# Kernel tuning notes

Hardware: AMD Instinct MI355X
Metric: run time of the kernel (lower is better)

## Reference

```python
import jax, jax.numpy as jnp
import numpy as np

N = 1048576
N_GRID = 256
DX = 1.0 / N_GRID
INV_DX = float(N_GRID)
DT = 2e-5
P_VOL = (DX * 0.5) ** 2
P_RHO = 1.0
P_MASS = P_VOL * P_RHO
E_MOD = 1000.0
NU = 0.2
MU_0 = E_MOD / (2.0 * (1.0 + NU))
LAM_0 = E_MOD * NU / ((1.0 + NU) * (1.0 - 2.0 * NU))
GRAVITY = 50.0


def setup_inputs() -> dict:
    key = jax.random.key(0)
    k = jax.random.split(key, 5)
    x = 0.1 + 0.8 * jax.random.uniform(k[0], (N, 2), dtype=jnp.float32)
    v = 0.1 * jax.random.normal(k[1], (N, 2), dtype=jnp.float32)
    C = 0.5 * jax.random.normal(k[2], (N, 2, 2), dtype=jnp.float32)
    F = jnp.eye(2, dtype=jnp.float32)[None] + 0.1 * jax.random.normal(k[3], (N, 2, 2), dtype=jnp.float32)
    material = jax.random.randint(k[4], (N,), 0, 3, dtype=jnp.int32)
    Jp = jnp.ones((N,), dtype=jnp.float32)
    return {"x": x, "v": v, "C": C, "F": F, "material": material, "Jp": Jp}


def reference(x, v, C, F, material, Jp):
    dt, inv_dx, dx = DT, INV_DX, DX
    base = jnp.floor(x * inv_dx - 0.5).astype(jnp.int32)          # [N,2]
    fx = x * inv_dx - base.astype(x.dtype)                        # [N,2]
    # quadratic B-spline weights, stacked over the 3 taps -> [3,N,2]
    w = jnp.stack([0.5 * (1.5 - fx) ** 2,
                   0.75 - (fx - 1.0) ** 2,
                   0.5 * (fx - 0.5) ** 2], axis=0)

    # deformation gradient update
    F = F + dt * jnp.einsum('nij,njk->nik', C, F)

    h = jnp.exp(10.0 * (1.0 - Jp))
    h = jnp.where(material == 1, 0.3, h)
    mu = jnp.where(material == 0, 0.0, MU_0 * h)
    lam = LAM_0 * h

    # per-particle 2x2 SVD (original pads to 3x3 and slices back)
    U, sig, Vh = jnp.linalg.svd(F)

    # snow plasticity: clamp singular values, track Jp
    clamped = jnp.clip(sig, 1.0 - 2.5e-2, 1.0 + 4.5e-3)
    is_snow = material == 2
    Jp = jnp.where(is_snow, Jp * jnp.prod(sig / clamped, axis=-1), Jp)
    sig = jnp.where(is_snow[:, None], clamped, sig)

    J = jnp.prod(sig, axis=-1)
    eye2 = jnp.eye(2, dtype=x.dtype)
    F_fluid = eye2[None] * jnp.sqrt(J)[:, None, None]             # J^(1/n_dim), n_dim=2
    F_snow = jnp.einsum('nij,nj,njk->nik', U, sig, Vh)
    F = jnp.where((material == 0)[:, None, None], F_fluid,
                  jnp.where(is_snow[:, None, None], F_snow, F))

    R = jnp.einsum('nij,njk->nik', U, Vh)
    stress = (2.0 * mu[:, None, None] * jnp.einsum('nij,nkj->nik', F - R, F)
              + eye2[None] * (lam * J * (J - 1.0))[:, None, None])
    stress = (-dt * P_VOL * 4.0 * inv_dx ** 2) * stress
    affine = stress + P_MASS * C                                   # [N,2,2]

    # ---- P2G scatter over the 3x3 stencil (vectorized over 9 taps) ----
    offs = jnp.array([[i, j] for i in range(3) for j in range(3)], dtype=jnp.int32)  # [9,2]
    weight = w[offs[:, 0], :, 0] * w[offs[:, 1], :, 1]             # [9,N]
    target = base[None, :, :] + offs[:, None, :]                   # [9,N,2]
    idx = target[..., 0] * N_GRID + target[..., 1]                 # [9,N]
    flat_idx = idx.reshape(-1)
    NG2 = N_GRID * N_GRID

    v_add = P_MASS * v - jnp.einsum('nij,nj->ni', affine, x)       # [N,2]
    grid_v = jax.ops.segment_sum((weight[..., None] * v_add[None]).reshape(-1, 2),
                                 flat_idx, num_segments=NG2).reshape(N_GRID, N_GRID, 2)
    grid_affine = jax.ops.segment_sum((weight[..., None, None] * affine[None]).reshape(-1, 4),
                                      flat_idx, num_segments=NG2).reshape(N_GRID, N_GRID, 2, 2)
    grid_m = jax.ops.segment_sum((weight * P_MASS).reshape(-1),
                                 flat_idx, num_segments=NG2).reshape(N_GRID, N_GRID)

    grid_x = jnp.stack(jnp.meshgrid(jnp.arange(N_GRID), jnp.arange(N_GRID), indexing='ij'),
                       axis=-1).astype(x.dtype) * dx               # [G,G,2]
    grid_v = grid_v + jnp.einsum('abij,abj->abi', grid_affine, grid_x)

    # grid ops: momentum -> velocity, gravity, boundary clamps
    m = grid_m[..., None]
    grid_v = jnp.where(m > 0, grid_v / jnp.maximum(m, 1e-12), grid_v)
    grid_v = grid_v.at[:, :, 1].add(-dt * GRAVITY)
    grid_v = grid_v.at[:3, :, 0].max(0.0)
    grid_v = grid_v.at[-2:, :, 0].min(0.0)
    grid_v = grid_v.at[:, :3, 1].max(0.0)
    grid_v = grid_v.at[:, -2:, 1].min(0.0)

    # ---- G2P gather ----
    gvf = grid_v.reshape(NG2, 2)
    g_v = gvf[idx]                                                 # [9,N,2]
    new_v = jnp.sum(weight[..., None] * g_v, axis=0)               # [N,2]
    pos = target.astype(x.dtype) * dx                              # [9,N,2]
    new_C = jnp.sum(weight[..., None, None] * g_v[..., :, None] * pos[..., None, :], axis=0)
    new_C = (new_C - new_v[..., None] * x[:, None, :]) * (4.0 * inv_dx ** 2)

    x = x + dt * new_v
    return (x, new_v, new_C, F, material, Jp)
```

## Files before the change

kernel.cpp:

```cpp
#include <hip/hip_runtime.h>

#define NG 256
#define NG2 (NG*NG)
#define NREP 8

constexpr float DX      = 1.0f / 256.0f;
constexpr float INV_DX  = 256.0f;
constexpr float DT      = 2e-5f;
constexpr float P_VOL   = (1.0f/512.0f) * (1.0f/512.0f);
constexpr float P_MASS  = P_VOL;
constexpr float MU_0    = 1000.0f / (2.0f * 1.2f);
constexpr float LAM_0   = 1000.0f * 0.2f / (1.2f * 0.6f);
constexpr float GRAV    = 50.0f;

__device__ __forceinline__ int bin_of(float px, float py) {
    int bx = (int)floorf(px * INV_DX - 0.5f);
    int by = (int)floorf(py * INV_DX - 0.5f);
    bx = min(max(bx, 0), NG - 1);
    by = min(max(by, 0), NG - 1);
    return (bx << 8) | by;
}

__device__ __forceinline__ float bw(float t) {
    float at = fabsf(t);
    float a  = fmaxf(1.5f - at, 0.0f);
    float w1 = 0.75f - t * t;
    float w2 = 0.5f * a * a;
    return (at < 0.5f) ? w1 : w2;
}


__global__ __launch_bounds__(256) void binrank_kernel(
    const float* __restrict__ x, int* __restrict__ counts8,
    unsigned char* __restrict__ rank, int n)
{
    int i = blockIdx.x * blockDim.x + threadIdx.x;
    if (i >= n) return;
    float2 p = ((const float2*)x)[i];
    int b = bin_of(p.x, p.y);
    int rep = (i >> 8) & (NREP - 1);
    rank[i] = (unsigned char)atomicAdd(&counts8[rep * NG2 + b], 1);
}

__global__ __launch_bounds__(256) void scan1_kernel(
    const int* __restrict__ counts8, uint2* __restrict__ offs8,
    int* __restrict__ starts, int* __restrict__ bsum)
{
    __shared__ int tmp[256];
    int t = threadIdx.x, blk = blockIdx.x;
    int b = blk * 256 + t;

    int c0 = counts8[0*NG2 + b], c1 = counts8[1*NG2 + b];
    int c2 = counts8[2*NG2 + b], c3 = counts8[3*NG2 + b];
    int c4 = counts8[4*NG2 + b], c5 = counts8[5*NG2 + b];
    int c6 = counts8[6*NG2 + b], c7 = counts8[7*NG2 + b];
    int o1 = c0, o2 = o1+c1, o3 = o2+c2, o4 = o3+c3;
    int o5 = o4+c4, o6 = o5+c5, o7 = o6+c6;
    int total = o7 + c7;
    uint2 packed;
    packed.x = (unsigned)(o1 << 8) | ((unsigned)o2 << 16) | ((unsigned)o3 << 24);
    packed.y = (unsigned)o4 | ((unsigned)o5 << 8) | ((unsigned)o6 << 16) | ((unsigned)o7 << 24);
    offs8[b] = packed;

    tmp[t] = total;
    __syncthreads();
    #pragma unroll
    for (int off = 1; off < 256; off <<= 1) {
        int add = (t >= off) ? tmp[t - off] : 0;
        __syncthreads();
        tmp[t] += add;
        __syncthreads();
    }
    starts[b] = tmp[t] - total;
    if (t == 255) bsum[blk] = tmp[255];
}

__global__ __launch_bounds__(256) void scan2_kernel(int* __restrict__ bsum)
{
    __shared__ int tmp[256];
    int t = threadIdx.x;
    int v = bsum[t];
    tmp[t] = v;
    __syncthreads();
    #pragma unroll
    for (int off = 1; off < 256; off <<= 1) {
        int add = (t >= off) ? tmp[t - off] : 0;
        __syncthreads();
        tmp[t] += add;
        __syncthreads();
    }
    bsum[t] = tmp[t] - v;
}

__global__ __launch_bounds__(256) void scan3_kernel(
    int* __restrict__ starts, const int* __restrict__ bsum, int n)
{
    int i = blockIdx.x * blockDim.x + threadIdx.x;
    if (i < NG2) starts[i] += bsum[i >> 8];
    if (i == 0) starts[NG2] = n;
}


__global__ __launch_bounds__(256) void compute_scatter_kernel(
    const float* __restrict__ x, const float* __restrict__ v,
    const float* __restrict__ C, const float* __restrict__ F,
    const int* __restrict__ mat, const float* __restrict__ Jp,
    const int* __restrict__ starts, const uint2* __restrict__ offs8,
    const unsigned char* __restrict__ rank,
    float4* __restrict__ srec,
    float4* __restrict__ F_out4, float* __restrict__ mat_out, float* __restrict__ Jp_out,
    int n)
{
    int i = blockIdx.x * blockDim.x + threadIdx.x;
    if (i >= n) return;

    float2 xp = ((const float2*)x)[i];
    float px = xp.x, py = xp.y;

    int bin = bin_of(px, py);
    int rep = (i >> 8) & (NREP - 1);
    uint2 o8 = offs8[bin];
    int sb = starts[bin];
    int rk = (int)rank[i];

    float2 vp = ((const float2*)v)[i];
    float4 Cp = ((const float4*)C)[i];
    float4 Fp = ((const float4*)F)[i];
    int    m  = mat[i];
    float  jp = Jp[i];

    float C00 = Cp.x, C01 = Cp.y, C10 = Cp.z, C11 = Cp.w;
    float a = Fp.x, b = Fp.y, c = Fp.z, d = Fp.w;

    float na = a + DT*(C00*a + C01*c);
    float nb = b + DT*(C00*b + C01*d);
    float nc = c + DT*(C10*a + C11*c);
    float nd = d + DT*(C10*b + C11*d);
    a = na; b = nb; c = nc; d = nd;

    float h = expf(10.0f * (1.0f - jp));
    if (m == 1) h = 0.3f;
    float mu  = (m == 0) ? 0.0f : MU_0 * h;
    float lam = LAM_0 * h;

    float S00 = a*a + c*c, S01 = a*b + c*d, S11 = b*b + d*d;
    float mh = 0.5f*(S00 + S11), dh = 0.5f*(S00 - S11);
    float delta = sqrtf(dh*dh + S01*S01);
    float sig1 = sqrtf(fmaxf(mh + delta, 0.0f));
    float sig2 = sqrtf(fmaxf(mh - delta, 0.0f));
    float e0, e1;
    if (dh >= 0.0f) { e0 = delta + dh; e1 = S01; }
    else            { e0 = S01;        e1 = delta - dh; }
    float elen = sqrtf(e0*e0 + e1*e1);
    float vc, vs;
    if (elen > 1e-30f) { float il = 1.0f/elen; vc = e0*il; vs = e1*il; }
    else               { vc = 1.0f; vs = 0.0f; }
    float inv1 = 1.0f / fmaxf(sig1, 1e-30f);
    float inv2 = 1.0f / fmaxf(sig2, 1e-30f);
    float u1x = ( a*vc + b*vs) * inv1, u1y = ( c*vc + d*vs) * inv1;
    float u2x = (-a*vs + b*vc) * inv2, u2y = (-c*vs + d*vc) * inv2;

    if (m == 2) {
        float c1 = fminf(fmaxf(sig1, 1.0f - 2.5e-2f), 1.0f + 4.5e-3f);
        float c2 = fminf(fmaxf(sig2, 1.0f - 2.5e-2f), 1.0f + 4.5e-3f);
        jp = jp * (sig1 / c1) * (sig2 / c2);
        sig1 = c1; sig2 = c2;
    }
    float J = sig1 * sig2;

    if (m == 0) {
        float s = sqrtf(J);
        a = s; b = 0.0f; c = 0.0f; d = s;
    } else if (m == 2) {
        a = sig1*u1x*vc - sig2*u2x*vs;
        b = sig1*u1x*vs + sig2*u2x*vc;
        c = sig1*u1y*vc - sig2*u2y*vs;
        d = sig1*u1y*vs + sig2*u2y*vc;
    }
    float R00 = u1x*vc - u2x*vs, R01 = u1x*vs + u2x*vc;
    float R10 = u1y*vc - u2y*vs, R11 = u1y*vs + u2y*vc;

    float k2mu = 2.0f * mu;
    float fr00 = a - R00, fr01 = b - R01, fr10 = c - R10, fr11 = d - R11;
    float ljj  = lam * J * (J - 1.0f);
    float st00 = k2mu*(fr00*a + fr01*b) + ljj;
    float st01 = k2mu*(fr00*c + fr01*d);
    float st10 = k2mu*(fr10*a + fr11*b);
    float st11 = k2mu*(fr10*c + fr11*d) + ljj;
    const float coef = -DT * P_VOL * 4.0f * INV_DX * INV_DX;
    float A00 = coef*st00 + P_MASS*C00;
    float A01 = coef*st01 + P_MASS*C01;
    float A10 = coef*st10 + P_MASS*C10;
    float A11 = coef*st11 + P_MASS*C11;

    float bx_ = P_MASS*vp.x - (A00*px + A01*py);
    float by_ = P_MASS*vp.y - (A10*px + A11*py);

    unsigned offv = (rep < 4 ? (o8.x >> (8*rep)) : (o8.y >> (8*(rep-4)))) & 255u;
    int sidx = sb + (int)offv + rk;
    srec[2*sidx]     = make_float4(px * INV_DX, py * INV_DX, bx_, by_);
    srec[2*sidx + 1] = make_float4(A00, A01, A10, A11);

    F_out4[i]  = make_float4(a, b, c, d);
    mat_out[i] = (float)m;
    Jp_out[i]  = jp;
}

__global__ __launch_bounds__(256) void gather_grid_kernel(
    const float4* __restrict__ srec, const int* __restrict__ starts,
    float2* __restrict__ gv)
{
    int bid  = blockIdx.x;
    int swz  = (bid & 7) * (4096 / 8) + (bid >> 3);
    int gtid  = swz * 256 + threadIdx.x;
    int cell  = gtid >> 4;
    int slice = gtid & 15;
    int gi = cell >> 8, gj = cell & (NG - 1);

    float fgi = (float)gi, fgj = (float)gj;
    float posx = fgi * DX, posy = fgj * DX;
    float msum = 0.0f, mvx = 0.0f, mvy = 0.0f;

    int j0 = max(gj - 2, 0);

    int sArr[3], eArr[3];
    #pragma unroll
    for (int t3 = 0; t3 < 3; ++t3) {
        int bi = gi - 2 + t3;
        bool valid = (bi >= 0);
        int row = (valid ? bi : 0) << 8;
        sArr[t3] = valid ? starts[row + j0] : 0;
        eArr[t3] = valid ? starts[row + gj + 1] : 0;
    }

    #pragma unroll
    for (int t3 = 0; t3 < 3; ++t3) {
        int s = sArr[t3], e = eArr[t3];
        for (int k = s + slice; k < e; k += 32) {
            float4 r0 = srec[2*k];
            float4 r1 = srec[2*k + 1];
            int k2 = k + 16;
            bool sec = (k2 < e);
            float4 q0, q1;
            if (sec) { q0 = srec[2*k2]; q1 = srec[2*k2 + 1]; }
            float w = bw(r0.x - fgi) * bw(r0.y - fgj);
            msum += w;
            mvx  += w * (r0.z + r1.x * posx + r1.y * posy);
            mvy  += w * (r0.w + r1.z * posx + r1.w * posy);
            if (sec) {
                float w2 = bw(q0.x - fgi) * bw(q0.y - fgj);
                msum += w2;
                mvx  += w2 * (q0.z + q1.x * posx + q1.y * posy);
                mvy  += w2 * (q0.w + q1.z * posx + q1.w * posy);
            }
        }
    }

    #pragma unroll
    for (int off = 1; off < 16; off <<= 1) {
        msum += __shfl_xor(msum, off);
        mvx  += __shfl_xor(mvx,  off);
        mvy  += __shfl_xor(mvy,  off);
    }

    if (slice == 0) {
        float mass = msum * P_MASS;
        float vx = mvx, vy = mvy;
        if (mass > 0.0f) {
            float im = 1.0f / fmaxf(mass, 1e-12f);
            vx *= im; vy *= im;
        }
        vy -= DT * GRAV;
        if (gi < 3)      vx = fmaxf(vx, 0.0f);
        if (gi >= NG-2)  vx = fminf(vx, 0.0f);
        if (gj < 3)      vy = fmaxf(vy, 0.0f);
        if (gj >= NG-2)  vy = fminf(vy, 0.0f);
        gv[cell] = make_float2(vx, vy);
    }
}

__global__ __launch_bounds__(256) void g2p_kernel(
    const float* __restrict__ x, const float2* __restrict__ gv,
    float* __restrict__ x_out, float* __restrict__ v_out, float* __restrict__ C_out,
    int n)
{
    int i = blockIdx.x * blockDim.x + threadIdx.x;
    if (i >= n) return;

    float2 xp = ((const float2*)x)[i];
    float px = xp.x, py = xp.y;
    float bxf = floorf(px * INV_DX - 0.5f), byf = floorf(py * INV_DX - 0.5f);
    float fx = px * INV_DX - bxf, fy = py * INV_DX - byf;
    float wxs[3] = { 0.5f*(1.5f-fx)*(1.5f-fx), 0.75f-(fx-1.0f)*(fx-1.0f), 0.5f*(fx-0.5f)*(fx-0.5f) };
    float wys[3] = { 0.5f*(1.5f-fy)*(1.5f-fy), 0.75f-(fy-1.0f)*(fy-1.0f), 0.5f*(fy-0.5f)*(fy-0.5f) };
    int bix = (int)bxf, biy = (int)byf;

    float nvx = 0.0f, nvy = 0.0f;
    float c00 = 0.0f, c01 = 0.0f, c10 = 0.0f, c11 = 0.0f;
    #pragma unroll
    for (int ii = 0; ii < 3; ++ii) {
        float posx = (bxf + (float)ii) * DX;
        int rowbase = (bix + ii) * NG + biy;
        #pragma unroll
        for (int jj = 0; jj < 3; ++jj) {
            float w = wxs[ii] * wys[jj];
            float posy = (byf + (float)jj) * DX;
            float2 g = gv[rowbase + jj];
            nvx += w * g.x; nvy += w * g.y;
            c00 += w * g.x * posx; c01 += w * g.x * posy;
            c10 += w * g.y * posx; c11 += w * g.y * posy;
        }
    }
    const float K = 4.0f * INV_DX * INV_DX;
    c00 = (c00 - nvx * px) * K; c01 = (c01 - nvx * py) * K;
    c10 = (c10 - nvy * px) * K; c11 = (c11 - nvy * py) * K;

    ((float2*)x_out)[i] = make_float2(px + DT * nvx, py + DT * nvy);
    ((float2*)v_out)[i] = make_float2(nvx, nvy);
    ((float4*)C_out)[i] = make_float4(c00, c01, c10, c11);
}

extern "C" void kernel_launch(void* const* d_in, const int* in_sizes, int n_in,
                              void* d_out, int out_size, void* d_ws, size_t ws_size,
                              hipStream_t stream) {
    const float* x   = (const float*)d_in[0];
    const float* v   = (const float*)d_in[1];
    const float* C   = (const float*)d_in[2];
    const float* F   = (const float*)d_in[3];
    const int*   mat = (const int*)d_in[4];
    const float* Jp  = (const float*)d_in[5];

    int n = in_sizes[0] / 2;

    float* out     = (float*)d_out;
    float* x_out   = out;
    float* v_out   = out + (size_t)2*n;
    float* C_out   = out + (size_t)4*n;
    float* F_out   = out + (size_t)8*n;
    float* mat_out = out + (size_t)12*n;
    float* Jp_out  = out + (size_t)13*n;

    float4* srec = (float4*)out;

    int blocks = (n + 255) / 256;

    char* ws = (char*)d_ws;
    size_t off = 0;
    int*   counts8 = (int*)(ws + off);  off += (size_t)NG2 * NREP * 4;
    int*   starts  = (int*)(ws + off);  off += (size_t)(NG2 + 1) * 4;
    uint2* offs8   = (uint2*)(ws + off); off += (size_t)NG2 * 8;
    int*   bsum    = (int*)(ws + off);  off += 256 * 4;
    unsigned char* rank = (unsigned char*)(ws + off); off += (size_t)n;
    off = (off + 63) & ~(size_t)63;
    float2* gv     = (float2*)(ws + off); off += (size_t)NG2 * 8;

    hipMemsetAsync(counts8, 0, (size_t)NG2 * NREP * 4, stream);
    binrank_kernel<<<blocks, 256, 0, stream>>>(x, counts8, rank, n);
    scan1_kernel<<<NG2/256, 256, 0, stream>>>(counts8, offs8, starts, bsum);
    scan2_kernel<<<1, 256, 0, stream>>>(bsum);
    scan3_kernel<<<NG2/256, 256, 0, stream>>>(starts, bsum, n);
    compute_scatter_kernel<<<blocks, 256, 0, stream>>>(x, v, C, F, mat, Jp,
                                                       starts, offs8, rank, srec,
                                                       (float4*)F_out, mat_out, Jp_out, n);
    gather_grid_kernel<<<(NG2*16)/256, 256, 0, stream>>>(srec, starts, gv);
    g2p_kernel<<<blocks, 256, 0, stream>>>(x, gv, x_out, v_out, C_out, n);
}
```

Measured before the change: 129.5 us.

## Compress sorted particle records to 16 bytes with fp16 and quantized offsets

The sorted particle record shrinks from two float4s to one uint4. Fractional cell positions are stored as 16-bit fixed point and the affine and momentum terms as half2, all expressed relative to the particle's base cell with mass factored out. The gather kernel now works out the tap offset from per-column bin boundaries instead of absolute positions, halving the bytes read per particle and dropping the dual-record unroll. The cost is precision loss from fp16 affine and momentum values, which may change results beyond tolerance.

```diff
diff --git a/kernel.cpp b/kernel.cpp
--- a/kernel.cpp
+++ b/kernel.cpp
@@ -1,4 +1,5 @@
 #include <hip/hip_runtime.h>
+#include <hip/hip_fp16.h>
 
 #define NG 256
 #define NG2 (NG*NG)
@@ -12,6 +13,8 @@
 constexpr float MU_0    = 1000.0f / (2.0f * 1.2f);
 constexpr float LAM_0   = 1000.0f * 0.2f / (1.2f * 0.6f);
 constexpr float GRAV    = 50.0f;
+constexpr float KA      = -DT * 4.0f * INV_DX * INV_DX;
+constexpr float MINMS   = 1e-12f / P_MASS;
 
 __device__ __forceinline__ int bin_of(float px, float py) {
     int bx = (int)floorf(px * INV_DX - 0.5f);
@@ -27,6 +30,17 @@
     float w1 = 0.75f - t * t;
     float w2 = 0.5f * a * a;
     return (at < 0.5f) ? w1 : w2;
+}
+
+__device__ __forceinline__ unsigned pack_h2(float a, float b) {
+    union { __half2 h; unsigned u; } cv;
+    cv.h = __floats2half2_rn(a, b);
+    return cv.u;
+}
+__device__ __forceinline__ float2 unpack_h2(unsigned u) {
+    union { __half2 h; unsigned u; } cv;
+    cv.u = u;
+    return __half22float2(cv.h);
 }
 
 
@@ -107,7 +121,7 @@
     const int* __restrict__ mat, const float* __restrict__ Jp,
     const int* __restrict__ starts, const uint2* __restrict__ offs8,
     const unsigned char* __restrict__ rank,
-    float4* __restrict__ srec,
+    uint4* __restrict__ srec,
     float4* __restrict__ F_out4, float* __restrict__ mat_out, float* __restrict__ Jp_out,
     int n)
 {
@@ -187,19 +201,30 @@
     float st01 = k2mu*(fr00*c + fr01*d);
     float st10 = k2mu*(fr10*a + fr11*b);
     float st11 = k2mu*(fr10*c + fr11*d) + ljj;
-    const float coef = -DT * P_VOL * 4.0f * INV_DX * INV_DX;
-    float A00 = coef*st00 + P_MASS*C00;
-    float A01 = coef*st01 + P_MASS*C01;
-    float A10 = coef*st10 + P_MASS*C10;
-    float A11 = coef*st11 + P_MASS*C11;
-
-    float bx_ = P_MASS*vp.x - (A00*px + A01*py);
-    float by_ = P_MASS*vp.y - (A10*px + A11*py);
+
+    float A00 = KA*st00 + C00;
+    float A01 = KA*st01 + C01;
+    float A10 = KA*st10 + C10;
+    float A11 = KA*st11 + C11;
+
+    float bxf = floorf(px * INV_DX - 0.5f), byf = floorf(py * INV_DX - 0.5f);
+    float fracx = px * INV_DX - bxf - 0.5f;
+    float fracy = py * INV_DX - byf - 0.5f;
+    float bppx = vp.x - DX * (A00*fracx + A01*fracy);
+    float bppy = vp.y - DX * (A10*fracx + A11*fracy);
+
+    unsigned qx = (unsigned)fminf(fracx * 65536.0f, 65535.0f);
+    unsigned qy = (unsigned)fminf(fracy * 65536.0f, 65535.0f);
 
     unsigned offv = (rep < 4 ? (o8.x >> (8*rep)) : (o8.y >> (8*(rep-4)))) & 255u;
     int sidx = sb + (int)offv + rk;
-    srec[2*sidx]     = make_float4(px * INV_DX, py * INV_DX, bx_, by_);
-    srec[2*sidx + 1] = make_float4(A00, A01, A10, A11);
+
+    uint4 rec;
+    rec.x = qx | (qy << 16);
+    rec.y = pack_h2(bppx, bppy);
+    rec.z = pack_h2(A00, A01);
+    rec.w = pack_h2(A10, A11);
+    srec[sidx] = rec;
 
     F_out4[i]  = make_float4(a, b, c, d);
     mat_out[i] = (float)m;
@@ -207,7 +232,7 @@
 }
 
 __global__ __launch_bounds__(256) void gather_grid_kernel(
-    const float4* __restrict__ srec, const int* __restrict__ starts,
+    const uint4* __restrict__ srec, const int* __restrict__ starts,
     float2* __restrict__ gv)
 {
     int bid  = blockIdx.x;
@@ -217,42 +242,42 @@
     int slice = gtid & 15;
     int gi = cell >> 8, gj = cell & (NG - 1);
 
-    float fgi = (float)gi, fgj = (float)gj;
-    float posx = fgi * DX, posy = fgj * DX;
     float msum = 0.0f, mvx = 0.0f, mvy = 0.0f;
 
-    int j0 = max(gj - 2, 0);
-
-    int sArr[3], eArr[3];
+    int b0[4], b1[4], b2[4];
+    #pragma unroll
+    for (int c = 0; c < 4; ++c) {
+        int col = gj - 2 + c;
+        int cc = col < 0 ? 0 : col;
+        int bi;
+        bi = gi - 2; b0[c] = (bi >= 0) ? starts[(bi << 8) + cc] : 0;
+        bi = gi - 1; b1[c] = (bi >= 0) ? starts[(bi << 8) + cc] : 0;
+        bi = gi;     b2[c] = starts[(bi << 8) + cc];
+    }
+
     #pragma unroll
     for (int t3 = 0; t3 < 3; ++t3) {
-        int bi = gi - 2 + t3;
-        bool valid = (bi >= 0);
-        int row = (valid ? bi : 0) << 8;
-        sArr[t3] = valid ? starts[row + j0] : 0;
-        eArr[t3] = valid ? starts[row + gj + 1] : 0;
-    }
-
-    #pragma unroll
-    for (int t3 = 0; t3 < 3; ++t3) {
-        int s = sArr[t3], e = eArr[t3];
-        for (int k = s + slice; k < e; k += 32) {
-            float4 r0 = srec[2*k];
-            float4 r1 = srec[2*k + 1];
-            int k2 = k + 16;
-            bool sec = (k2 < e);
-            float4 q0, q1;
-            if (sec) { q0 = srec[2*k2]; q1 = srec[2*k2 + 1]; }
-            float w = bw(r0.x - fgi) * bw(r0.y - fgj);
+        int s, e, m1, m2;
+        if (t3 == 0)      { s = b0[0]; m1 = b0[1]; m2 = b0[2]; e = b0[3]; }
+        else if (t3 == 1) { s = b1[0]; m1 = b1[1]; m2 = b1[2]; e = b1[3]; }
+        else              { s = b2[0]; m1 = b2[1]; m2 = b2[2]; e = b2[3]; }
+        float basex = (float)(t3 - 2);
+        float dgx   = -(basex + 0.5f) * DX;
+
+        for (int k = s + slice; k < e; k += 16) {
+            uint4 r = srec[k];
+            int cc = (k >= m1) + (k >= m2);
+            float fx = (float)(r.x & 0xffffu) * (1.0f/65536.0f);
+            float fy = (float)(r.x >> 16)     * (1.0f/65536.0f);
+            float basey = (float)cc - 2.0f;
+            float dgy   = -(basey + 0.5f) * DX;
+            float w = bw(basex + 0.5f + fx) * bw(basey + 0.5f + fy);
+            float2 bb = unpack_h2(r.y);
+            float2 a0 = unpack_h2(r.z);
+            float2 a1 = unpack_h2(r.w);
             msum += w;
-            mvx  += w * (r0.z + r1.x * posx + r1.y * posy);
-            mvy  += w * (r0.w + r1.z * posx + r1.w * posy);
-            if (sec) {
-                float w2 = bw(q0.x - fgi) * bw(q0.y - fgj);
-                msum += w2;
-                mvx  += w2 * (q0.z + q1.x * posx + q1.y * posy);
-                mvy  += w2 * (q0.w + q1.z * posx + q1.w * posy);
-            }
+            mvx  += w * (bb.x + a0.x * dgx + a0.y * dgy);
+            mvy  += w * (bb.y + a1.x * dgx + a1.y * dgy);
         }
     }
 
@@ -264,10 +289,9 @@
     }
 
     if (slice == 0) {
-        float mass = msum * P_MASS;
         float vx = mvx, vy = mvy;
-        if (mass > 0.0f) {
-            float im = 1.0f / fmaxf(mass, 1e-12f);
+        if (msum > 0.0f) {
+            float im = 1.0f / fmaxf(msum, MINMS);
             vx *= im; vy *= im;
         }
         vy -= DT * GRAV;
@@ -340,7 +364,7 @@
     float* mat_out = out + (size_t)12*n;
     float* Jp_out  = out + (size_t)13*n;
 
-    float4* srec = (float4*)out;
+    uint4* srec = (uint4*)out;
 
     int blocks = (n + 255) / 256;
 
```

After: 128.3 us. No clear change (-1.0%).
